# Kernel tuning notes

Measured on AMD Instinct MI355X. Metric: run time of the kernel, lower is better.

The kernel has to match this reference:

```python
import jax, jax.numpy as jnp
import numpy as np

B = 4096
LATENT = 32
BASE_C = 32
NUM_LAYERS = 4
# channel schedule: in halves each layer except last keeps width
_INS = [32, 16, 8, 4]
_OUTS = [16, 8, 4, 4]


def setup_inputs() -> dict:
    key = jax.random.key(0)
    ks = jax.random.split(key, 4 + 3 * NUM_LAYERS)
    inp = {
        "x": jax.random.normal(ks[0], (B, LATENT), dtype=jnp.float32),
        "fc_w": jax.random.normal(ks[1], (BASE_C, LATENT), dtype=jnp.float32) * 0.1,
        "fc_b": jnp.zeros((BASE_C,), dtype=jnp.float32),
        "const": jax.random.normal(ks[2], (1, BASE_C, 4, 4), dtype=jnp.float32),
    }
    for i in range(NUM_LAYERS):
        cin, cout = _INS[i], _OUTS[i]
        k0, k1, k2 = jax.random.split(ks[4 + i], 3)
        inp[f"conv_w{i}"] = jax.random.normal(k0, (cout, cin, 3, 3), dtype=jnp.float32) * (1.0 / np.sqrt(cin * 9))
        inp[f"mod_w{i}"] = jax.random.normal(k1, (cin, BASE_C), dtype=jnp.float32) * 0.1
        inp[f"mod_b{i}"] = jnp.ones((cin,), dtype=jnp.float32)
    return inp


def _style_conv(h, style, conv_w, mod_w, mod_b):
    # h: [B, Cin, H, W], style: [B, 32]
    b, cin, H, W = h.shape
    cout = conv_w.shape[0]
    s = style @ mod_w.T + mod_b                        # [B, Cin]
    w = conv_w[None] * s[:, None, :, None, None]       # [B, Cout, Cin, 3, 3]
    demod = jax.lax.rsqrt(jnp.sum(w * w, axis=(2, 3, 4)) + 1e-8)  # [B, Cout]
    w = w * demod[:, :, None, None, None]
    w = w.reshape(b * cout, cin, 3, 3)
    hg = h.reshape(1, b * cin, H, W)
    y = jax.lax.conv_general_dilated(
        hg, w, window_strides=(1, 1), padding=((1, 1), (1, 1)),
        feature_group_count=b, dimension_numbers=("NCHW", "OIHW", "NCHW"))
    y = y.reshape(b, cout, H, W)
    # bilinear x2 upsample, align_corners=False (half-pixel centers)
    return jax.image.resize(y, (b, cout, 2 * H, 2 * W), method="bilinear")


def reference(x, fc_w, fc_b, const,
              conv_w0, mod_w0, mod_b0,
              conv_w1, mod_w1, mod_b1,
              conv_w2, mod_w2, mod_b2,
              conv_w3, mod_w3, mod_b3):
    style = x @ fc_w.T + fc_b                          # [B, BASE_C]
    out = jnp.broadcast_to(const, (x.shape[0],) + const.shape[1:])
    layers = [(conv_w0, mod_w0, mod_b0), (conv_w1, mod_w1, mod_b1),
              (conv_w2, mod_w2, mod_b2), (conv_w3, mod_w3, mod_b3)]
    feats = []
    for cw, mw, mb in layers:
        out = _style_conv(out, style, cw, mw, mb)
        feats.append(out)
    return tuple(feats)
```

## Files before the change

kernel.cpp:

```cpp
#include <hip/hip_runtime.h>

#define TPB 256

constexpr int M_STYLE = 8880;
constexpr int M_S     = 8912;
constexpr int M_D     = 8972;
constexpr int LDSF    = 9008;

template<int CIN, int COUT, int H, int R>
__device__ __forceinline__ void conv3x3(const float* __restrict__ hp,
                                        const float* __restrict__ wb,
                                        float* __restrict__ c, int tid)
{
    constexpr int W = H, HS = H + 2;
    constexpr int LW = (W==4)?2:((W==8)?3:((W==16)?4:5));
    constexpr int LC = (COUT==16)?4:((COUT==8)?3:2);
    constexpr int WS = CIN*9 + 1;
    const int xx = tid & (W-1);
    const int co = (tid >> LW) & (COUT-1);
    const int y0 = (tid >> (LW+LC)) * R;
    float acc[R];
#pragma unroll
    for (int r = 0; r < R; r++) acc[r] = 0.f;
    const float* wco = wb + co*WS;
#pragma unroll
    for (int ci = 0; ci < CIN; ci++) {
        const float* hc = hp + ci*HS*HS + xx;
#pragma unroll
        for (int dx = 0; dx < 3; dx++) {
            float col[R+2];
#pragma unroll
            for (int r = 0; r < R+2; r++) col[r] = hc[(y0+r)*HS + dx];
#pragma unroll
            for (int dy = 0; dy < 3; dy++) {
                const float wv = wco[ci*9 + dy*3 + dx];
#pragma unroll
                for (int r = 0; r < R; r++) acc[r] = fmaf(wv, col[r+dy], acc[r]);
            }
        }
    }
#pragma unroll
    for (int r = 0; r < R; r++) c[co*H*W + (y0+r)*W + xx] = acc[r];
}

template<int COUT, int H, bool LAST>
__device__ __forceinline__ void upsample(const float* __restrict__ c,
                                         const float* __restrict__ dmv,
                                         const float* __restrict__ snext,
                                         float* __restrict__ hnext,
                                         float* __restrict__ gout, int tid)
{
    constexpr int W = H;
    constexpr int LW = (W==4)?2:((W==8)?3:((W==16)?4:5));
    constexpr int LC = (COUT==16)?4:((COUT==8)?3:2);
    constexpr int STRIPS = 256/(W*COUT);
    constexpr int KQ = H / STRIPS;
    constexpr int NS = 2*H + 2;
    const int p  = tid & (W-1);
    const int co = (tid >> LW) & (COUT-1);
    const int k0 = (tid >> (LW+LC)) * KQ;
    const float dm = dmv[co];
    float sn = 0.f;
    if constexpr (!LAST) sn = snext[co];
    const int xm = (p==0) ? 0 : p-1;
    const int xp = (p==W-1) ? W-1 : p+1;
    const float* cc = c + co*H*W;
#pragma unroll
    for (int k = k0; k < k0+KQ; k++) {
        const int km = (k==0) ? 0 : k-1;
        const int kp = (k==H-1) ? H-1 : k+1;
        const float am = cc[km*W+xm], a0 = cc[km*W+p], ap = cc[km*W+xp];
        const float bm = cc[k *W+xm], b0 = cc[k *W+p], bp = cc[k *W+xp];
        const float em = cc[kp*W+xm], e0 = cc[kp*W+p], ep = cc[kp*W+xp];
        const float tm0 = 0.25f*am + 0.75f*bm, t00 = 0.25f*a0 + 0.75f*b0, tp0 = 0.25f*ap + 0.75f*bp;
        const float tm1 = 0.75f*bm + 0.25f*em, t01 = 0.75f*b0 + 0.25f*e0, tp1 = 0.75f*bp + 0.25f*ep;
        const float o00 = (0.25f*tm0 + 0.75f*t00) * dm;
        const float o01 = (0.75f*t00 + 0.25f*tp0) * dm;
        const float o10 = (0.25f*tm1 + 0.75f*t01) * dm;
        const float o11 = (0.75f*t01 + 0.25f*tp1) * dm;
        float* g = gout + co*(4*H*W) + (2*k)*(2*W) + 2*p;
        *(float2*)g          = make_float2(o00, o01);
        *(float2*)(g + 2*W)  = make_float2(o10, o11);
        if constexpr (!LAST) {
            float* hb = hnext + co*NS*NS + (2*k+1)*NS + (2*p+1);
            hb[0]    = o00*sn;  hb[1]    = o01*sn;
            hb[NS]   = o10*sn;  hb[NS+1] = o11*sn;
        }
    }
}

template<int C, int NS>
__device__ __forceinline__ void zero_halo(float* hn, int tid)
{
    for (int j = tid; j < C*NS*NS; j += TPB) {
        const int r = j % (NS*NS);
        const int y = r / NS, x2 = r % NS;
        if (y == 0 || y == NS-1 || x2 == 0 || x2 == NS-1) hn[j] = 0.f;
    }
}

template<int CIN, int COUT>
__device__ __forceinline__ void load_w(const float* __restrict__ g, float* __restrict__ wb, int tid)
{
    constexpr int N = COUT*CIN*9;
    for (int j = tid; j < N; j += TPB) {
        const int co = j / (CIN*9);
        wb[co*(CIN*9+1) + (j - co*(CIN*9))] = g[j];
    }
}

__global__ void __launch_bounds__(TPB)
decoder_kernel(const float* __restrict__ x,   const float* __restrict__ fc_w,
               const float* __restrict__ fc_b,const float* __restrict__ cst,
               const float* __restrict__ cw0, const float* __restrict__ mw0, const float* __restrict__ mb0,
               const float* __restrict__ cw1, const float* __restrict__ mw1, const float* __restrict__ mb1,
               const float* __restrict__ cw2, const float* __restrict__ mw2, const float* __restrict__ mb2,
               const float* __restrict__ cw3, const float* __restrict__ mw3, const float* __restrict__ mb3,
               float* __restrict__ f0, float* __restrict__ f1,
               float* __restrict__ f2, float* __restrict__ f3)
{
    __shared__ float lds[LDSF];
    const int tid = threadIdx.x;
    const int b   = blockIdx.x;

    if (tid < 32) {
        const float* xr = x + (size_t)b*32;
        const float* fw = fc_w + tid*32;
        float acc = fc_b[tid];
#pragma unroll
        for (int k = 0; k < 32; k++) acc = fmaf(xr[k], fw[k], acc);
        lds[M_STYLE + tid] = acc;
    }
    __syncthreads();

    if (tid < 60) {
        int ci; const float* mwp; const float* mbp;
        if (tid < 32)      { ci = tid;      mwp = mw0; mbp = mb0; }
        else if (tid < 48) { ci = tid - 32; mwp = mw1; mbp = mb1; }
        else if (tid < 56) { ci = tid - 48; mwp = mw2; mbp = mb2; }
        else               { ci = tid - 56; mwp = mw3; mbp = mb3; }
        mwp += ci*32;
        float acc = mbp[ci];
#pragma unroll
        for (int k = 0; k < 32; k++) acc = fmaf(lds[M_STYLE + k], mwp[k], acc);
        lds[M_S + tid] = acc;
    }
    load_w<32,16>(cw0, &lds[1856], tid);
    __syncthreads();

    {
        const int g = tid >> 3, l = tid & 7;
        int co, cin; const float* wp; const float* sp;
        if (g < 16)      { co = g;      cin = 32; wp = cw0; sp = &lds[M_S];      }
        else if (g < 24) { co = g - 16; cin = 16; wp = cw1; sp = &lds[M_S + 32]; }
        else if (g < 28) { co = g - 24; cin = 8;  wp = cw2; sp = &lds[M_S + 48]; }
        else             { co = g - 28; cin = 4;  wp = cw3; sp = &lds[M_S + 56]; }
        wp += co*cin*9;
        float acc = 0.f;
        for (int e = l; e < cin*9; e += 8) {
            const int ci = e / 9;
            const float wv = wp[e] * sp[ci];
            acc = fmaf(wv, wv, acc);
        }
        acc += __shfl_xor(acc, 1);
        acc += __shfl_xor(acc, 2);
        acc += __shfl_xor(acc, 4);
        if (l == 0) lds[M_D + g] = rsqrtf(acc + 1e-8f);
    }
    for (int j = tid; j < 1152; j += TPB) {
        const int ci = j / 36, r = j - ci*36, y = r / 6, x2 = r - y*6;
        float v = 0.f;
        if (y >= 1 && y <= 4 && x2 >= 1 && x2 <= 4)
            v = lds[M_S + ci] * cst[ci*16 + (y-1)*4 + (x2-1)];
        lds[j] = v;
    }
    __syncthreads();

    conv3x3<32,16,4,1>(&lds[0], &lds[1856], &lds[1600], tid);
    __syncthreads();
    upsample<16,4,false>(&lds[1600], &lds[M_D], &lds[M_S + 32], &lds[0],
                         f0 + (size_t)b*1024, tid);
    zero_halo<16,10>(&lds[0], tid);
    load_w<16,8>(cw1, &lds[3104], tid);
    __syncthreads();

    conv3x3<16,8,8,2>(&lds[0], &lds[3104], &lds[2592], tid);
    __syncthreads();
    upsample<8,8,false>(&lds[2592], &lds[M_D + 16], &lds[M_S + 48], &lds[0],
                        f1 + (size_t)b*2048, tid);
    zero_halo<8,18>(&lds[0], tid);
    load_w<8,4>(cw2, &lds[3104], tid);
    __syncthreads();

    conv3x3<8,4,16,4>(&lds[0], &lds[3104], &lds[4624], tid);
    __syncthreads();
    upsample<4,16,false>(&lds[4624], &lds[M_D + 24], &lds[M_S + 56], &lds[0],
                         f2 + (size_t)b*4096, tid);
    zero_halo<4,34>(&lds[0], tid);
    load_w<4,4>(cw3, &lds[8720], tid);
    __syncthreads();

    conv3x3<4,4,32,16>(&lds[0], &lds[8720], &lds[4624], tid);
    __syncthreads();
    upsample<4,32,true>(&lds[4624], &lds[M_D + 28], nullptr, nullptr,
                        f3 + (size_t)b*16384, tid);
}

extern "C" void kernel_launch(void* const* d_in, const int* in_sizes, int n_in,
                              void* d_out, int out_size, void* d_ws, size_t ws_size,
                              hipStream_t stream)
{
    const float* x    = (const float*)d_in[0];
    const float* fc_w = (const float*)d_in[1];
    const float* fc_b = (const float*)d_in[2];
    const float* cst  = (const float*)d_in[3];
    const float* cw0  = (const float*)d_in[4];
    const float* mw0  = (const float*)d_in[5];
    const float* mb0  = (const float*)d_in[6];
    const float* cw1  = (const float*)d_in[7];
    const float* mw1  = (const float*)d_in[8];
    const float* mb1  = (const float*)d_in[9];
    const float* cw2  = (const float*)d_in[10];
    const float* mw2  = (const float*)d_in[11];
    const float* mb2  = (const float*)d_in[12];
    const float* cw3  = (const float*)d_in[13];
    const float* mw3  = (const float*)d_in[14];
    const float* mb3  = (const float*)d_in[15];
    float* out = (float*)d_out;

    const int Bn = in_sizes[0] / 32;
    float* f0 = out;
    float* f1 = f0 + (size_t)Bn*1024;
    float* f2 = f1 + (size_t)Bn*2048;
    float* f3 = f2 + (size_t)Bn*4096;

    decoder_kernel<<<dim3(Bn), dim3(TPB), 0, stream>>>(
        x, fc_w, fc_b, cst,
        cw0, mw0, mb0, cw1, mw1, mb1, cw2, mw2, mb2, cw3, mw3, mb3,
        f0, f1, f2, f3);
}
```

Baseline: 494.2 us.

## Vectorize conv and upsample with 4-wide register tiles and padded LDS layouts

Rewrites the per-layer 3x3 conv so each thread computes a 4-column by R-row tile from a register window loaded with float4/float2 LDS reads. Weights are repacked to a 12-float stride for vector loads. Conv output now goes to a row-padded buffer with replicated edges so the bilinear upsample can read vectors and write 8-wide float4 outputs. Other changes: the halo zeroing touches only border cells, the LDS map is re-laid out with a larger footprint, and launch bounds now request 4 blocks per CU. The trade-off is that fewer threads are active in the early layers, and register pressure is higher.

```diff
diff --git a/kernel.cpp b/kernel.cpp
--- a/kernel.cpp
+++ b/kernel.cpp
@@ -2,114 +2,168 @@
 
 #define TPB 256
 
-constexpr int M_STYLE = 8880;
-constexpr int M_S     = 8912;
-constexpr int M_D     = 8972;
-constexpr int LDSF    = 9008;
-
-template<int CIN, int COUT, int H, int R>
-__device__ __forceinline__ void conv3x3(const float* __restrict__ hp,
-                                        const float* __restrict__ wb,
-                                        float* __restrict__ c, int tid)
-{
-    constexpr int W = H, HS = H + 2;
-    constexpr int LW = (W==4)?2:((W==8)?3:((W==16)?4:5));
-    constexpr int LC = (COUT==16)?4:((COUT==8)?3:2);
-    constexpr int WS = CIN*9 + 1;
-    const int xx = tid & (W-1);
-    const int co = (tid >> LW) & (COUT-1);
-    const int y0 = (tid >> (LW+LC)) * R;
-    float acc[R];
-#pragma unroll
-    for (int r = 0; r < R; r++) acc[r] = 0.f;
-    const float* wco = wb + co*WS;
-#pragma unroll
-    for (int ci = 0; ci < CIN; ci++) {
-        const float* hc = hp + ci*HS*HS + xx;
-#pragma unroll
-        for (int dx = 0; dx < 3; dx++) {
-            float col[R+2];
-#pragma unroll
-            for (int r = 0; r < R+2; r++) col[r] = hc[(y0+r)*HS + dx];
-#pragma unroll
-            for (int dy = 0; dy < 3; dy++) {
-                const float wv = wco[ci*9 + dy*3 + dx];
-#pragma unroll
-                for (int r = 0; r < R; r++) acc[r] = fmaf(wv, col[r+dy], acc[r]);
+constexpr int O_C0    = 2304;
+constexpr int O_W0    = 2816;
+constexpr int O_W1    = 2816;
+constexpr int O_C1    = 4384;
+constexpr int O_W2    = 5152;
+constexpr int O_C2    = 5552;
+constexpr int O_W3    = 5184;
+constexpr int O_C3    = 5392;
+constexpr int M_STYLE = 10000;
+constexpr int M_S     = 10032;
+constexpr int M_D     = 10092;
+constexpr int LDSF    = 10124;
+
+template<int CIN, int COUT, int H, int R, int HS>
+__device__ __forceinline__ void conv4(const float* __restrict__ hp,
+                                      const float* __restrict__ wb,
+                                      float* __restrict__ c, int tid)
+{
+    constexpr int XT = H/4, RS = H/R, NT = COUT*RS*XT;
+    constexpr int WS = CIN*12 + 4;
+    constexpr int PL = HS*HS;
+    constexpr int CS = H + 4;
+    constexpr int CP = H * CS;
+    if (tid < NT) {
+        const int t  = tid % XT;
+        const int rs = (tid / XT) % RS;
+        const int co = tid / (XT*RS);
+        const int y0 = rs * R;
+        const int x0 = 4*t;
+        const float* wrow = wb + co*WS;
+        float acc[R][4];
+#pragma unroll
+        for (int r = 0; r < R; r++) { acc[r][0]=acc[r][1]=acc[r][2]=acc[r][3]=0.f; }
+        for (int ci = 0; ci < CIN; ci++) {
+            const float* bp = hp + ci*PL + y0*HS + x0;
+            float win[R+2][6];
+#pragma unroll
+            for (int rr = 0; rr < R+2; rr++) {
+                const float4 a = *(const float4*)(bp + rr*HS);
+                const float2 b = *(const float2*)(bp + rr*HS + 4);
+                win[rr][0]=a.x; win[rr][1]=a.y; win[rr][2]=a.z; win[rr][3]=a.w;
+                win[rr][4]=b.x; win[rr][5]=b.y;
             }
-        }
-    }
-#pragma unroll
-    for (int r = 0; r < R; r++) c[co*H*W + (y0+r)*W + xx] = acc[r];
-}
-
-template<int COUT, int H, bool LAST>
-__device__ __forceinline__ void upsample(const float* __restrict__ c,
-                                         const float* __restrict__ dmv,
-                                         const float* __restrict__ snext,
-                                         float* __restrict__ hnext,
-                                         float* __restrict__ gout, int tid)
-{
-    constexpr int W = H;
-    constexpr int LW = (W==4)?2:((W==8)?3:((W==16)?4:5));
-    constexpr int LC = (COUT==16)?4:((COUT==8)?3:2);
-    constexpr int STRIPS = 256/(W*COUT);
-    constexpr int KQ = H / STRIPS;
-    constexpr int NS = 2*H + 2;
-    const int p  = tid & (W-1);
-    const int co = (tid >> LW) & (COUT-1);
-    const int k0 = (tid >> (LW+LC)) * KQ;
-    const float dm = dmv[co];
-    float sn = 0.f;
-    if constexpr (!LAST) sn = snext[co];
-    const int xm = (p==0) ? 0 : p-1;
-    const int xp = (p==W-1) ? W-1 : p+1;
-    const float* cc = c + co*H*W;
-#pragma unroll
-    for (int k = k0; k < k0+KQ; k++) {
-        const int km = (k==0) ? 0 : k-1;
-        const int kp = (k==H-1) ? H-1 : k+1;
-        const float am = cc[km*W+xm], a0 = cc[km*W+p], ap = cc[km*W+xp];
-        const float bm = cc[k *W+xm], b0 = cc[k *W+p], bp = cc[k *W+xp];
-        const float em = cc[kp*W+xm], e0 = cc[kp*W+p], ep = cc[kp*W+xp];
-        const float tm0 = 0.25f*am + 0.75f*bm, t00 = 0.25f*a0 + 0.75f*b0, tp0 = 0.25f*ap + 0.75f*bp;
-        const float tm1 = 0.75f*bm + 0.25f*em, t01 = 0.75f*b0 + 0.25f*e0, tp1 = 0.75f*bp + 0.25f*ep;
-        const float o00 = (0.25f*tm0 + 0.75f*t00) * dm;
-        const float o01 = (0.75f*t00 + 0.25f*tp0) * dm;
-        const float o10 = (0.25f*tm1 + 0.75f*t01) * dm;
-        const float o11 = (0.75f*t01 + 0.25f*tp1) * dm;
-        float* g = gout + co*(4*H*W) + (2*k)*(2*W) + 2*p;
-        *(float2*)g          = make_float2(o00, o01);
-        *(float2*)(g + 2*W)  = make_float2(o10, o11);
-        if constexpr (!LAST) {
-            float* hb = hnext + co*NS*NS + (2*k+1)*NS + (2*p+1);
-            hb[0]    = o00*sn;  hb[1]    = o01*sn;
-            hb[NS]   = o10*sn;  hb[NS+1] = o11*sn;
-        }
-    }
-}
-
-template<int C, int NS>
-__device__ __forceinline__ void zero_halo(float* hn, int tid)
-{
-    for (int j = tid; j < C*NS*NS; j += TPB) {
-        const int r = j % (NS*NS);
-        const int y = r / NS, x2 = r % NS;
-        if (y == 0 || y == NS-1 || x2 == 0 || x2 == NS-1) hn[j] = 0.f;
+            const float4 wA = *(const float4*)(wrow + ci*12);
+            const float4 wB = *(const float4*)(wrow + ci*12 + 4);
+            const float  w8 = wrow[ci*12 + 8];
+            const float wt[9] = {wA.x,wA.y,wA.z,wA.w,wB.x,wB.y,wB.z,wB.w,w8};
+#pragma unroll
+            for (int r = 0; r < R; r++)
+#pragma unroll
+                for (int dy = 0; dy < 3; dy++)
+#pragma unroll
+                    for (int dx = 0; dx < 3; dx++) {
+                        const float wv = wt[dy*3+dx];
+#pragma unroll
+                        for (int j = 0; j < 4; j++)
+                            acc[r][j] = fmaf(wv, win[r+dy][j+dx], acc[r][j]);
+                    }
+        }
+        float* crow = c + co*CP + y0*CS + x0 + 1;
+#pragma unroll
+        for (int r = 0; r < R; r++) {
+#pragma unroll
+            for (int j = 0; j < 4; j++) crow[r*CS + j] = acc[r][j];
+            if (t == 0)     crow[r*CS - 1] = acc[r][0];
+            if (t == XT-1)  crow[r*CS + 4] = acc[r][3];
+        }
+    }
+}
+
+template<int COUT, int H, int KQ, bool LAST, int HSN>
+__device__ __forceinline__ void up4(const float* __restrict__ c,
+                                    const float* __restrict__ dmv,
+                                    const float* __restrict__ snext,
+                                    float* __restrict__ hnext,
+                                    float* __restrict__ gout, int tid)
+{
+    constexpr int XT = H/4, KS = H/KQ, NT = COUT*KS*XT;
+    constexpr int CS = H + 4, CP = H*CS;
+    constexpr int PLN = HSN*HSN;
+    if (tid < NT) {
+        const int t  = tid % XT;
+        const int ks = (tid / XT) % KS;
+        const int co = tid / (XT*KS);
+        const int k0 = ks*KQ;
+        const float dm = dmv[co];
+        float sn = 0.f;
+        if constexpr (!LAST) sn = snext[co];
+        const float* cb = c + co*CP + 4*t;
+        float he[KQ+2][4], ho[KQ+2][4];
+#pragma unroll
+        for (int i = 0; i < KQ+2; i++) {
+            int r = k0 - 1 + i; r = r < 0 ? 0 : (r > H-1 ? H-1 : r);
+            const float4 a = *(const float4*)(cb + r*CS);
+            const float2 b = *(const float2*)(cb + r*CS + 4);
+            const float w0=a.x*dm, w1=a.y*dm, w2=a.z*dm, w3=a.w*dm, w4=b.x*dm, w5=b.y*dm;
+            he[i][0]=0.25f*w0+0.75f*w1;  ho[i][0]=0.75f*w1+0.25f*w2;
+            he[i][1]=0.25f*w1+0.75f*w2;  ho[i][1]=0.75f*w2+0.25f*w3;
+            he[i][2]=0.25f*w2+0.75f*w3;  ho[i][2]=0.75f*w3+0.25f*w4;
+            he[i][3]=0.25f*w3+0.75f*w4;  ho[i][3]=0.75f*w4+0.25f*w5;
+        }
+        float* gbase = gout + co*(4*H*H) + 8*t;
+#pragma unroll
+        for (int kk = 0; kk < KQ; kk++) {
+            const int k = k0 + kk;
+            float r0[8], r1[8];
+#pragma unroll
+            for (int j = 0; j < 4; j++) {
+                r0[2*j]   = 0.25f*he[kk][j]   + 0.75f*he[kk+1][j];
+                r0[2*j+1] = 0.25f*ho[kk][j]   + 0.75f*ho[kk+1][j];
+                r1[2*j]   = 0.75f*he[kk+1][j] + 0.25f*he[kk+2][j];
+                r1[2*j+1] = 0.75f*ho[kk+1][j] + 0.25f*ho[kk+2][j];
+            }
+            *(float4*)(gbase + (2*k)*(2*H))       = make_float4(r0[0],r0[1],r0[2],r0[3]);
+            *(float4*)(gbase + (2*k)*(2*H) + 4)   = make_float4(r0[4],r0[5],r0[6],r0[7]);
+            *(float4*)(gbase + (2*k+1)*(2*H))     = make_float4(r1[0],r1[1],r1[2],r1[3]);
+            *(float4*)(gbase + (2*k+1)*(2*H) + 4) = make_float4(r1[4],r1[5],r1[6],r1[7]);
+            if constexpr (!LAST) {
+                float* hb = hnext + co*PLN + (2*k+1)*HSN + 8*t + 1;
+#pragma unroll
+                for (int j = 0; j < 8; j++) hb[j] = r0[j]*sn;
+                hb += HSN;
+#pragma unroll
+                for (int j = 0; j < 8; j++) hb[j] = r1[j]*sn;
+            }
+        }
+    }
+}
+
+template<int C, int DH, int HSN>
+__device__ __forceinline__ void zhalo(float* hp, int tid)
+{
+    constexpr int NR = C*HSN*2;
+    for (int j = tid; j < NR; j += TPB) {
+        const int ch = j / (2*HSN), rr = j % (2*HSN);
+        const int row = (rr < HSN) ? 0 : DH+1;
+        hp[ch*HSN*HSN + row*HSN + (rr % HSN)] = 0.f;
+    }
+    constexpr int NC = C*DH*2;
+    for (int j = tid; j < NC; j += TPB) {
+        const int ch = j / (2*DH), rr = j % (2*DH);
+        const int col = (rr < DH) ? 0 : DH+1;
+        hp[ch*HSN*HSN + (1 + (rr % DH))*HSN + col] = 0.f;
     }
 }
 
 template<int CIN, int COUT>
-__device__ __forceinline__ void load_w(const float* __restrict__ g, float* __restrict__ wb, int tid)
+__device__ __forceinline__ void load_w(const float* __restrict__ g,
+                                       float* __restrict__ wb, int tid)
 {
     constexpr int N = COUT*CIN*9;
+    constexpr int WS = CIN*12 + 4;
     for (int j = tid; j < N; j += TPB) {
         const int co = j / (CIN*9);
-        wb[co*(CIN*9+1) + (j - co*(CIN*9))] = g[j];
-    }
-}
-
-__global__ void __launch_bounds__(TPB)
+        const int r  = j - co*(CIN*9);
+        const int ci = r / 9;
+        const int k  = r - ci*9;
+        wb[co*WS + ci*12 + k] = g[j];
+    }
+}
+
+__global__ void __launch_bounds__(TPB, 4)
 decoder_kernel(const float* __restrict__ x,   const float* __restrict__ fc_w,
                const float* __restrict__ fc_b,const float* __restrict__ cst,
                const float* __restrict__ cw0, const float* __restrict__ mw0, const float* __restrict__ mb0,
@@ -145,7 +199,7 @@
         for (int k = 0; k < 32; k++) acc = fmaf(lds[M_STYLE + k], mwp[k], acc);
         lds[M_S + tid] = acc;
     }
-    load_w<32,16>(cw0, &lds[1856], tid);
+    load_w<32,16>(cw0, &lds[O_W0], tid);
     __syncthreads();
 
     {
@@ -167,43 +221,43 @@
         acc += __shfl_xor(acc, 4);
         if (l == 0) lds[M_D + g] = rsqrtf(acc + 1e-8f);
     }
-    for (int j = tid; j < 1152; j += TPB) {
-        const int ci = j / 36, r = j - ci*36, y = r / 6, x2 = r - y*6;
+    for (int j = tid; j < 2048; j += TPB) {
+        const int ci = j >> 6, r = j & 63, y = r >> 3, xx = r & 7;
         float v = 0.f;
-        if (y >= 1 && y <= 4 && x2 >= 1 && x2 <= 4)
-            v = lds[M_S + ci] * cst[ci*16 + (y-1)*4 + (x2-1)];
+        if (y >= 1 && y <= 4 && xx >= 1 && xx <= 4)
+            v = lds[M_S + ci] * cst[ci*16 + (y-1)*4 + (xx-1)];
         lds[j] = v;
     }
     __syncthreads();
 
-    conv3x3<32,16,4,1>(&lds[0], &lds[1856], &lds[1600], tid);
-    __syncthreads();
-    upsample<16,4,false>(&lds[1600], &lds[M_D], &lds[M_S + 32], &lds[0],
+    conv4<32,16,4,1,8>(&lds[0], &lds[O_W0], &lds[O_C0], tid);
+    __syncthreads();
+    up4<16,4,1,false,12>(&lds[O_C0], &lds[M_D], &lds[M_S+32], &lds[0],
                          f0 + (size_t)b*1024, tid);
-    zero_halo<16,10>(&lds[0], tid);
-    load_w<16,8>(cw1, &lds[3104], tid);
-    __syncthreads();
-
-    conv3x3<16,8,8,2>(&lds[0], &lds[3104], &lds[2592], tid);
-    __syncthreads();
-    upsample<8,8,false>(&lds[2592], &lds[M_D + 16], &lds[M_S + 48], &lds[0],
+    zhalo<16,8,12>(&lds[0], tid);
+    load_w<16,8>(cw1, &lds[O_W1], tid);
+    __syncthreads();
+
+    conv4<16,8,8,1,12>(&lds[0], &lds[O_W1], &lds[O_C1], tid);
+    __syncthreads();
+    up4<8,8,1,false,20>(&lds[O_C1], &lds[M_D+16], &lds[M_S+48], &lds[0],
                         f1 + (size_t)b*2048, tid);
-    zero_halo<8,18>(&lds[0], tid);
-    load_w<8,4>(cw2, &lds[3104], tid);
-    __syncthreads();
-
-    conv3x3<8,4,16,4>(&lds[0], &lds[3104], &lds[4624], tid);
-    __syncthreads();
-    upsample<4,16,false>(&lds[4624], &lds[M_D + 24], &lds[M_S + 56], &lds[0],
+    zhalo<8,16,20>(&lds[0], tid);
+    load_w<8,4>(cw2, &lds[O_W2], tid);
+    __syncthreads();
+
+    conv4<8,4,16,1,20>(&lds[0], &lds[O_W2], &lds[O_C2], tid);
+    __syncthreads();
+    up4<4,16,1,false,36>(&lds[O_C2], &lds[M_D+24], &lds[M_S+56], &lds[0],
                          f2 + (size_t)b*4096, tid);
-    zero_halo<4,34>(&lds[0], tid);
-    load_w<4,4>(cw3, &lds[8720], tid);
-    __syncthreads();
-
-    conv3x3<4,4,32,16>(&lds[0], &lds[8720], &lds[4624], tid);
-    __syncthreads();
-    upsample<4,32,true>(&lds[4624], &lds[M_D + 28], nullptr, nullptr,
-                        f3 + (size_t)b*16384, tid);
+    zhalo<4,32,36>(&lds[0], tid);
+    load_w<4,4>(cw3, &lds[O_W3], tid);
+    __syncthreads();
+
+    conv4<4,4,32,4,36>(&lds[0], &lds[O_W3], &lds[O_C3], tid);
+    __syncthreads();
+    up4<4,32,4,true,1>(&lds[O_C3], &lds[M_D+28], nullptr, nullptr,
+                       f3 + (size_t)b*16384, tid);
 }
 
 extern "C" void kernel_launch(void* const* d_in, const int* in_sizes, int n_in,
```

After: 755.3 us. 1.53x slower.
